# Performance work log

Measured on AMD Instinct MI355X. Metric: run time of the kernel, lower is better.

Reference implementation:

```python
import jax, jax.numpy as jnp
import numpy as np

B = 128   # number of graphs/molecules in batch
L = 1024  # padded max nodes per graph (dense dim of message_passing_matrix)
C = 16    # coefficient channels
N = 65536 # total nodes across batch


def setup_inputs() -> dict:
    key = jax.random.key(0)
    k1, k2, k3 = jax.random.split(key, 3)
    x = jax.random.normal(k1, (N, C), dtype=jnp.float32)
    message_passing_matrix = jax.random.normal(k2, (B, L, L), dtype=jnp.float32)
    coeffs_batch = jnp.sort(jax.random.randint(k3, (N,), 0, B)).astype(jnp.int64)
    return {"x": x, "message_passing_matrix": message_passing_matrix,
            "coeffs_batch": coeffs_batch}


def reference(x, message_passing_matrix, coeffs_batch):
    # to_dense_batch: scatter ragged node features into [B, L, C] padded tensor
    n, c = x.shape
    counts = jax.ops.segment_sum(jnp.ones((n,), jnp.int32), coeffs_batch,
                                 num_segments=B)          # [B] nodes per graph
    starts = jnp.cumsum(counts) - counts                  # [B] first index of each graph
    pos = jnp.arange(n) - starts[coeffs_batch]            # [N] position within graph
    dense = jnp.zeros((B, L, c), x.dtype).at[coeffs_batch, pos].set(x)  # [B,L,C]
    # batched message passing matmul
    y = jnp.einsum('bij,bjc->bic', message_passing_matrix, dense)       # [B,L,C]
    # y[mask]: gather valid rows back in original node order -> [N, C]
    return y[coeffs_batch, pos]
```

## Files before the change

### kernel.cpp

```cpp
#include <hip/hip_runtime.h>

#define L 1024
#define C 16
#define RT 64
#define KT 32
#define XSTR 1032

typedef __attribute__((ext_vector_type(8))) short short8v;
typedef __attribute__((ext_vector_type(4))) float f32x4;

static __device__ __forceinline__ short f2bf(float f) {
  unsigned u = __builtin_bit_cast(unsigned, f);
  u = (u + 0x7fffu + ((u >> 16) & 1u)) >> 16;
  return (short)u;
}

__global__ void starts_kernel(const int* __restrict__ batch, int n, int bp1,
                              int* __restrict__ starts) {
  int i = blockIdx.x * blockDim.x + threadIdx.x;
  if (i >= bp1) return;
  int lo = 0, hi = n;
  while (lo < hi) { int mid = (lo + hi) >> 1; if (batch[mid] < i) lo = mid + 1; else hi = mid; }
  starts[i] = lo;
}

__global__ __launch_bounds__(256) void mp_kernel(
    const float* __restrict__ x,
    const float* __restrict__ M,
    const int*   __restrict__ starts,
    float*       __restrict__ out)
{
  __shared__ short Xt[C * XSTR];

  const int b  = blockIdx.y;
  const int sb = starts[b];
  int cnt = starts[b + 1] - sb;
  if (cnt > L) cnt = L;
  const int r0 = blockIdx.x * RT;
  if (r0 >= cnt) return;

  const int njt  = (cnt + KT - 1) / KT;
  const int jmax = njt * KT;

  const float* xb = x + (size_t)sb * C;
  const int t = threadIdx.x;
  for (int j0 = t * 2; j0 < jmax; j0 += 512) {
    float4 va0, va1, vb0, vb1;
    const float4 fz = make_float4(0.f, 0.f, 0.f, 0.f);
    if (j0 < cnt) {
      va0 = *reinterpret_cast<const float4*>(xb + (size_t)j0 * C);
      va1 = *reinterpret_cast<const float4*>(xb + (size_t)j0 * C + 4);
      vb0 = *reinterpret_cast<const float4*>(xb + (size_t)j0 * C + 8);
      vb1 = *reinterpret_cast<const float4*>(xb + (size_t)j0 * C + 12);
    } else { va0 = fz; va1 = fz; vb0 = fz; vb1 = fz; }
    float4 wa0, wa1, wb0, wb1;
    if (j0 + 1 < cnt) {
      wa0 = *reinterpret_cast<const float4*>(xb + (size_t)(j0 + 1) * C);
      wa1 = *reinterpret_cast<const float4*>(xb + (size_t)(j0 + 1) * C + 4);
      wb0 = *reinterpret_cast<const float4*>(xb + (size_t)(j0 + 1) * C + 8);
      wb1 = *reinterpret_cast<const float4*>(xb + (size_t)(j0 + 1) * C + 12);
    } else { wa0 = fz; wa1 = fz; wb0 = fz; wb1 = fz; }
    const float av[16] = {va0.x,va0.y,va0.z,va0.w, va1.x,va1.y,va1.z,va1.w,
                          vb0.x,vb0.y,vb0.z,vb0.w, vb1.x,vb1.y,vb1.z,vb1.w};
    const float bv[16] = {wa0.x,wa0.y,wa0.z,wa0.w, wa1.x,wa1.y,wa1.z,wa1.w,
                          wb0.x,wb0.y,wb0.z,wb0.w, wb1.x,wb1.y,wb1.z,wb1.w};
    #pragma unroll
    for (int c = 0; c < C; ++c) {
      short2 p; p.x = f2bf(av[c]); p.y = f2bf(bv[c]);
      *reinterpret_cast<short2*>(&Xt[c * XSTR + j0]) = p;
    }
  }
  asm volatile("s_waitcnt lgkmcnt(0)" ::: "memory");
  __builtin_amdgcn_s_barrier();

  const int lane = t & 63;
  const int wv   = t >> 6;
  const int arow = r0 + (wv << 4) + (lane & 15);
  const int kc8  = (lane >> 4) << 3;
  const int bcol = lane & 15;
  const float* Mrow = M + (size_t)b * (L * L) + (size_t)arow * L + kc8;
  const short* Xrow = &Xt[bcol * XSTR + kc8];

  f32x4 acc = {0.f, 0.f, 0.f, 0.f};

  auto ldA = [&](int ks, float4& ra, float4& rb) {
    const float* p = Mrow + ks * KT;
    ra = *reinterpret_cast<const float4*>(p);
    rb = *reinterpret_cast<const float4*>(p + 4);
  };
  auto mk = [&](const float4& a, const float4& bq) {
    short8v v;
    v[0] = f2bf(a.x);  v[1] = f2bf(a.y);  v[2] = f2bf(a.z);  v[3] = f2bf(a.w);
    v[4] = f2bf(bq.x); v[5] = f2bf(bq.y); v[6] = f2bf(bq.z); v[7] = f2bf(bq.w);
    return v;
  };
  auto ldB = [&](int ks) {
    return *reinterpret_cast<const short8v*>(Xrow + ks * KT);
  };

  float4 A0, B0, A1, B1, A2, B2;
  ldA(0, A0, B0);
  if (njt > 1) ldA(1, A1, B1);
  if (njt > 2) ldA(2, A2, B2);

  for (int ks = 0; ks < njt; ks += 3) {
    {
      short8v bf = ldB(ks);
      acc = __builtin_amdgcn_mfma_f32_16x16x32_bf16(mk(A0, B0), bf, acc, 0, 0, 0);
      if (ks + 3 < njt) ldA(ks + 3, A0, B0);
    }
    if (ks + 1 < njt) {
      short8v bf = ldB(ks + 1);
      acc = __builtin_amdgcn_mfma_f32_16x16x32_bf16(mk(A1, B1), bf, acc, 0, 0, 0);
      if (ks + 4 < njt) ldA(ks + 4, A1, B1);
    }
    if (ks + 2 < njt) {
      short8v bf = ldB(ks + 2);
      acc = __builtin_amdgcn_mfma_f32_16x16x32_bf16(mk(A2, B2), bf, acc, 0, 0, 0);
      if (ks + 5 < njt) ldA(ks + 5, A2, B2);
    }
  }

  const int orow = r0 + (wv << 4) + ((lane >> 4) << 2);
  #pragma unroll
  for (int r = 0; r < 4; ++r) {
    const int gr = orow + r;
    if (gr < cnt)
      out[(size_t)(sb + gr) * C + bcol] = acc[r];
  }
}

extern "C" void kernel_launch(void* const* d_in, const int* in_sizes, int n_in,
                              void* d_out, int out_size, void* d_ws, size_t ws_size,
                              hipStream_t stream) {
  const float* x     = (const float*)d_in[0];
  const float* M     = (const float*)d_in[1];
  const int*   batch = (const int*)d_in[2];
  float*       out   = (float*)d_out;
  const int n_nodes  = in_sizes[2];
  const int B        = in_sizes[1] / (L * L);
  int* starts = (int*)d_ws;

  starts_kernel<<<1, 256, 0, stream>>>(batch, n_nodes, B + 1, starts);
  dim3 grid(L / RT, B);
  mp_kernel<<<grid, dim3(256), 0, stream>>>(x, M, starts, out);
}
```

Baseline: 51.11 us.

## Deepen M prefetch to eight tiles, remap block grid, parallelize starts computation

Raises the software prefetch depth for the M row loads from three to eight outstanding tiles, with clamped addresses and zero-padded X so the loop needs no bounds branches. The grid becomes 1D and is remapped so that consecutive blocks interleave eight graphs, and launch bounds request four blocks per CU. The starts computation changes from a single-block binary search to a per-node boundary scan over many blocks, and bf16 conversion uses the library intrinsic. The goal is more memory-level parallelism on the bandwidth-bound M stream, at the cost of more registers and redundant clamped loads at the tail.

```diff
diff --git a/kernel.cpp b/kernel.cpp
--- a/kernel.cpp
+++ b/kernel.cpp
@@ -1,30 +1,34 @@
 #include <hip/hip_runtime.h>
+#include <hip/hip_bf16.h>
 
 #define L 1024
 #define C 16
 #define RT 64
 #define KT 32
 #define XSTR 1032
+#define DEPTH 8
 
 typedef __attribute__((ext_vector_type(8))) short short8v;
 typedef __attribute__((ext_vector_type(4))) float f32x4;
 
 static __device__ __forceinline__ short f2bf(float f) {
-  unsigned u = __builtin_bit_cast(unsigned, f);
-  u = (u + 0x7fffu + ((u >> 16) & 1u)) >> 16;
-  return (short)u;
+  __hip_bfloat16 h = __float2bfloat16(f);
+  return __builtin_bit_cast(short, h);
+}
+static __device__ __forceinline__ int imin(int a, int b) { return a < b ? a : b; }
+
+__global__ void starts_kernel(const int* __restrict__ batch, int n, int nb,
+                              int* __restrict__ starts) {
+  int i = blockIdx.x * blockDim.x + threadIdx.x;
+  if (i >= n) return;
+  int cur  = batch[i];
+  int prev = (i == 0) ? -1 : batch[i - 1];
+  for (int g = prev + 1; g <= cur; ++g) starts[g] = i;
+  if (i == n - 1)
+    for (int g = cur + 1; g <= nb; ++g) starts[g] = n;
 }
 
-__global__ void starts_kernel(const int* __restrict__ batch, int n, int bp1,
-                              int* __restrict__ starts) {
-  int i = blockIdx.x * blockDim.x + threadIdx.x;
-  if (i >= bp1) return;
-  int lo = 0, hi = n;
-  while (lo < hi) { int mid = (lo + hi) >> 1; if (batch[mid] < i) lo = mid + 1; else hi = mid; }
-  starts[i] = lo;
-}
-
-__global__ __launch_bounds__(256) void mp_kernel(
+__global__ __launch_bounds__(256, 4) void mp_kernel(
     const float* __restrict__ x,
     const float* __restrict__ M,
     const int*   __restrict__ starts,
@@ -32,34 +36,39 @@
 {
   __shared__ short Xt[C * XSTR];
 
-  const int b  = blockIdx.y;
+  const int gid = blockIdx.x;
+  const int bx  = (gid >> 3) & 15;
+  const int b   = (gid & 7) | ((gid >> 7) << 3);
+
   const int sb = starts[b];
   int cnt = starts[b + 1] - sb;
   if (cnt > L) cnt = L;
-  const int r0 = blockIdx.x * RT;
+  const int r0 = bx * RT;
   if (r0 >= cnt) return;
 
-  const int njt  = (cnt + KT - 1) / KT;
-  const int jmax = njt * KT;
+  const int njt   = (cnt + KT - 1) / KT;
+  const int njtm1 = njt - 1;
+  const int njt3  = ((njt + DEPTH - 1) / DEPTH) * DEPTH;
+  const int jmax3 = njt3 * KT;
 
   const float* xb = x + (size_t)sb * C;
   const int t = threadIdx.x;
-  for (int j0 = t * 2; j0 < jmax; j0 += 512) {
-    float4 va0, va1, vb0, vb1;
+  for (int j0 = t * 2; j0 < jmax3; j0 += 512) {
     const float4 fz = make_float4(0.f, 0.f, 0.f, 0.f);
+    float4 va0 = fz, va1 = fz, vb0 = fz, vb1 = fz;
+    float4 wa0 = fz, wa1 = fz, wb0 = fz, wb1 = fz;
     if (j0 < cnt) {
       va0 = *reinterpret_cast<const float4*>(xb + (size_t)j0 * C);
       va1 = *reinterpret_cast<const float4*>(xb + (size_t)j0 * C + 4);
       vb0 = *reinterpret_cast<const float4*>(xb + (size_t)j0 * C + 8);
       vb1 = *reinterpret_cast<const float4*>(xb + (size_t)j0 * C + 12);
-    } else { va0 = fz; va1 = fz; vb0 = fz; vb1 = fz; }
-    float4 wa0, wa1, wb0, wb1;
+    }
     if (j0 + 1 < cnt) {
       wa0 = *reinterpret_cast<const float4*>(xb + (size_t)(j0 + 1) * C);
       wa1 = *reinterpret_cast<const float4*>(xb + (size_t)(j0 + 1) * C + 4);
       wb0 = *reinterpret_cast<const float4*>(xb + (size_t)(j0 + 1) * C + 8);
       wb1 = *reinterpret_cast<const float4*>(xb + (size_t)(j0 + 1) * C + 12);
-    } else { wa0 = fz; wa1 = fz; wb0 = fz; wb1 = fz; }
+    }
     const float av[16] = {va0.x,va0.y,va0.z,va0.w, va1.x,va1.y,va1.z,va1.w,
                           vb0.x,vb0.y,vb0.z,vb0.w, vb1.x,vb1.y,vb1.z,vb1.w};
     const float bv[16] = {wa0.x,wa0.y,wa0.z,wa0.w, wa1.x,wa1.y,wa1.z,wa1.w,
@@ -83,43 +92,32 @@
 
   f32x4 acc = {0.f, 0.f, 0.f, 0.f};
 
-  auto ldA = [&](int ks, float4& ra, float4& rb) {
-    const float* p = Mrow + ks * KT;
-    ra = *reinterpret_cast<const float4*>(p);
-    rb = *reinterpret_cast<const float4*>(p + 4);
-  };
-  auto mk = [&](const float4& a, const float4& bq) {
-    short8v v;
-    v[0] = f2bf(a.x);  v[1] = f2bf(a.y);  v[2] = f2bf(a.z);  v[3] = f2bf(a.w);
-    v[4] = f2bf(bq.x); v[5] = f2bf(bq.y); v[6] = f2bf(bq.z); v[7] = f2bf(bq.w);
-    return v;
-  };
-  auto ldB = [&](int ks) {
-    return *reinterpret_cast<const short8v*>(Xrow + ks * KT);
-  };
+#define LDA(s, ks) do { \
+    const float* p_ = Mrow + (size_t)imin((ks), njtm1) * KT; \
+    Aa##s = *reinterpret_cast<const float4*>(p_); \
+    Ab##s = *reinterpret_cast<const float4*>(p_ + 4); \
+  } while (0)
+#define MK(s) ({ short8v v_; \
+    v_[0]=f2bf(Aa##s.x); v_[1]=f2bf(Aa##s.y); v_[2]=f2bf(Aa##s.z); v_[3]=f2bf(Aa##s.w); \
+    v_[4]=f2bf(Ab##s.x); v_[5]=f2bf(Ab##s.y); v_[6]=f2bf(Ab##s.z); v_[7]=f2bf(Ab##s.w); v_; })
+#define STEP(s, kcur) do { \
+    short8v bf_ = *reinterpret_cast<const short8v*>(Xrow + (size_t)(kcur) * KT); \
+    acc = __builtin_amdgcn_mfma_f32_16x16x32_bf16(MK(s), bf_, acc, 0, 0, 0); \
+    LDA(s, (kcur) + DEPTH); \
+  } while (0)
 
-  float4 A0, B0, A1, B1, A2, B2;
-  ldA(0, A0, B0);
-  if (njt > 1) ldA(1, A1, B1);
-  if (njt > 2) ldA(2, A2, B2);
+  float4 Aa0, Ab0, Aa1, Ab1, Aa2, Ab2, Aa3, Ab3;
+  float4 Aa4, Ab4, Aa5, Ab5, Aa6, Ab6, Aa7, Ab7;
+  LDA(0, 0); LDA(1, 1); LDA(2, 2); LDA(3, 3);
+  LDA(4, 4); LDA(5, 5); LDA(6, 6); LDA(7, 7);
 
-  for (int ks = 0; ks < njt; ks += 3) {
-    {
-      short8v bf = ldB(ks);
-      acc = __builtin_amdgcn_mfma_f32_16x16x32_bf16(mk(A0, B0), bf, acc, 0, 0, 0);
-      if (ks + 3 < njt) ldA(ks + 3, A0, B0);
-    }
-    if (ks + 1 < njt) {
-      short8v bf = ldB(ks + 1);
-      acc = __builtin_amdgcn_mfma_f32_16x16x32_bf16(mk(A1, B1), bf, acc, 0, 0, 0);
-      if (ks + 4 < njt) ldA(ks + 4, A1, B1);
-    }
-    if (ks + 2 < njt) {
-      short8v bf = ldB(ks + 2);
-      acc = __builtin_amdgcn_mfma_f32_16x16x32_bf16(mk(A2, B2), bf, acc, 0, 0, 0);
-      if (ks + 5 < njt) ldA(ks + 5, A2, B2);
-    }
+  for (int kb = 0; kb < njt3; kb += DEPTH) {
+    STEP(0, kb + 0); STEP(1, kb + 1); STEP(2, kb + 2); STEP(3, kb + 3);
+    STEP(4, kb + 4); STEP(5, kb + 5); STEP(6, kb + 6); STEP(7, kb + 7);
   }
+#undef LDA
+#undef MK
+#undef STEP
 
   const int orow = r0 + (wv << 4) + ((lane >> 4) << 2);
   #pragma unroll
@@ -141,7 +139,6 @@
   const int B        = in_sizes[1] / (L * L);
   int* starts = (int*)d_ws;
 
-  starts_kernel<<<1, 256, 0, stream>>>(batch, n_nodes, B + 1, starts);
-  dim3 grid(L / RT, B);
-  mp_kernel<<<grid, dim3(256), 0, stream>>>(x, M, starts, out);
+  starts_kernel<<<(n_nodes + 255) / 256, 256, 0, stream>>>(batch, n_nodes, B, starts);
+  mp_kernel<<<dim3((L / RT) * B), dim3(256), 0, stream>>>(x, M, starts, out);
 }
```

New measurement: 49.26 us. 1.04x faster.
